# Optimization experiments

Measured on AMD Instinct MI355X. Metric: run time of the kernel, lower is better.

The kernel has to match this reference:

```python
import jax, jax.numpy as jnp
import numpy as np

B, N, C, H = 2, 2048, 1024, 16
D = C // H  # head_dim = 64
ROPE_THETA = 500000.0
INIT_STD = 0.02


def setup_inputs() -> dict:
    key = jax.random.key(0)
    ks = jax.random.split(key, 6)
    hidden_states = jax.random.normal(ks[0], (B, N, C), dtype=jnp.float32)
    # rotary embeddings: standard llama-style, built from rope_theta
    inv_freq = jnp.asarray(1.0 / (ROPE_THETA ** (np.arange(0, D, 2, dtype=np.float32) / D)), jnp.float32)
    freqs = jnp.outer(jnp.arange(N, dtype=jnp.float32), inv_freq)  # (N, D/2)
    emb = jnp.concatenate([freqs, freqs], axis=-1)  # (N, D)
    cos = jnp.broadcast_to(jnp.cos(emb)[None], (B, N, D))
    sin = jnp.broadcast_to(jnp.sin(emb)[None], (B, N, D))
    Wq = jax.random.normal(ks[1], (C, C), jnp.float32) * INIT_STD
    Wk = jax.random.normal(ks[2], (C, C), jnp.float32) * INIT_STD
    Wv = jax.random.normal(ks[3], (C, C), jnp.float32) * INIT_STD
    Wo = jax.random.normal(ks[4], (C, C), jnp.float32) * INIT_STD
    return {"hidden_states": hidden_states, "cos": cos, "sin": sin,
            "Wq": Wq, "Wk": Wk, "Wv": Wv, "Wo": Wo}


def _rotate_half(x):
    x1, x2 = x[..., : D // 2], x[..., D // 2 :]
    return jnp.concatenate((-x2, x1), axis=-1)


def reference(hidden_states, cos, sin, Wq, Wk, Wv, Wo):
    scaling = D ** -0.5
    # projections; W stored as (in, out) so y = x @ W
    q = (hidden_states @ Wq) * scaling
    k = hidden_states @ Wk
    v = hidden_states @ Wv
    q = q.reshape(B, N, H, D)
    k = k.reshape(B, N, H, D)
    v = v.reshape(B, N, H, D)
    # RoPE, cos/sin broadcast over heads: (B,N,1,D)
    c = cos[:, :, None, :]
    s = sin[:, :, None, :]
    q = q * c + _rotate_half(q) * s
    k = k * c + _rotate_half(k) * s
    # causal SDPA (q already scaled)
    scores = jnp.einsum("bqhd,bkhd->bhqk", q, k)  # (B,H,N,N)
    causal = jnp.tril(jnp.ones((N, N), dtype=bool))
    scores = jnp.where(causal[None, None], scores, jnp.finfo(scores.dtype).min)
    probs = jax.nn.softmax(scores, axis=-1)
    out = jnp.einsum("bhqk,bkhd->bqhd", probs, v).reshape(B, N, C)
    return out @ Wo
```

## Files before the change

kernel.cpp:

```cpp
#include <hip/hip_runtime.h>
#include <hip/hip_bf16.h>

typedef __hip_bfloat16 bf16;
typedef __attribute__((ext_vector_type(8))) short short8;
typedef __attribute__((ext_vector_type(4))) short short4v;
typedef __attribute__((ext_vector_type(4))) float f32x4;

#define BB 2
#define NN 2048
#define CC 1024
#define HH 16
#define DD 64
#define MM (BB*NN)
#define QKVN 3072
#define LOG2E 1.44269504088896340736f

__device__ __forceinline__ void glds16(const void* g, void* l) {
    __builtin_amdgcn_global_load_lds((const __attribute__((address_space(1))) void*)g,
                                     (__attribute__((address_space(3))) void*)l, 16, 0, 0);
}
__device__ __forceinline__ short pkbf(float x) { bf16 t = (bf16)x; return *(short*)&t; }

__global__ __launch_bounds__(256) void convert_f32_bf16(const float* __restrict__ in,
                                                        bf16* __restrict__ out) {
    int i = blockIdx.x * 256 + threadIdx.x;
    float4 v = ((const float4*)in)[i];
    short4v s;
    s.x = pkbf(v.x); s.y = pkbf(v.y); s.z = pkbf(v.z); s.w = pkbf(v.w);
    *((short4v*)out + i) = s;
}

__global__ __launch_bounds__(256) void transpose4(const float* __restrict__ W0,
                                                  const float* __restrict__ W1,
                                                  const float* __restrict__ W2,
                                                  const float* __restrict__ W3,
                                                  bf16* __restrict__ Wtqkv,
                                                  bf16* __restrict__ Wto) {
    __shared__ float t[32][33];
    const int z = blockIdx.z;
    const float* W = z == 0 ? W0 : (z == 1 ? W1 : (z == 2 ? W2 : W3));
    bf16* dst = z < 3 ? Wtqkv + (size_t)z * CC * CC : Wto;
    const int tx = threadIdx.x, ty = threadIdx.y;
    const int x0 = blockIdx.x * 32, y0 = blockIdx.y * 32;
    #pragma unroll
    for (int i = 0; i < 4; ++i)
        t[ty + i * 8][tx] = W[(size_t)(y0 + ty + i * 8) * CC + x0 + tx];
    __syncthreads();
    #pragma unroll
    for (int i = 0; i < 4; ++i)
        dst[(size_t)(x0 + ty + i * 8) * CC + y0 + tx] = (bf16)t[tx][ty + i * 8];
}

template<int Nn, int MODE>
__global__ __launch_bounds__(256) void gemm3(const bf16* __restrict__ A,
                                             const bf16* __restrict__ Bt,
                                             void* __restrict__ Cout,
                                             const float* __restrict__ cosp,
                                             const float* __restrict__ sinp,
                                             bf16* __restrict__ VtOut) {
    __shared__ __align__(16) bf16 As[2][128 * 32];
    __shared__ __align__(16) bf16 Bs[2][128 * 32];
    const int tid = threadIdx.x, lane = tid & 63, wid = tid >> 6;
    const int wr = wid >> 1, wc = wid & 1, l16 = lane & 15, lg = lane >> 4;
    const int n0 = blockIdx.x * 128, m0 = blockIdx.y * 128;

    f32x4 acc[4][4];
    #pragma unroll
    for (int i = 0; i < 4; ++i)
        #pragma unroll
        for (int j = 0; j < 4; ++j) acc[i][j] = {0.f, 0.f, 0.f, 0.f};

    const int issue0 = wid * 2;
    const int sr0 = (issue0 * 1024 + lane * 16) >> 6;
    const int sc0 = ((issue0 * 1024 + lane * 16) & 63) >> 1;
    const int sr1 = ((issue0 + 1) * 1024 + lane * 16) >> 6;
    const int sc1 = (((issue0 + 1) * 1024 + lane * 16) & 63) >> 1;

    auto stage = [&](int k0, int bufi) {
        glds16(&A [(size_t)(m0 + sr0) * 1024 + k0 + sc0], (char*)&As[bufi][0] + issue0 * 1024);
        glds16(&Bt[(size_t)(n0 + sr0) * 1024 + k0 + sc0], (char*)&Bs[bufi][0] + issue0 * 1024);
        glds16(&A [(size_t)(m0 + sr1) * 1024 + k0 + sc1], (char*)&As[bufi][0] + (issue0 + 1) * 1024);
        glds16(&Bt[(size_t)(n0 + sr1) * 1024 + k0 + sc1], (char*)&Bs[bufi][0] + (issue0 + 1) * 1024);
    };

    stage(0, 0);
    for (int t = 0; t < 32; ++t) {
        const int cur = t & 1;
        __syncthreads();
        if (t + 1 < 32) stage((t + 1) * 32, cur ^ 1);
        short8 af[4], bfr[4];
        #pragma unroll
        for (int i = 0; i < 4; ++i) af[i]  = *(const short8*)((char*)&As[cur][0] + (wr * 64 + i * 16 + l16) * 64 + lg * 16);
        #pragma unroll
        for (int j = 0; j < 4; ++j) bfr[j] = *(const short8*)((char*)&Bs[cur][0] + (wc * 64 + j * 16 + l16) * 64 + lg * 16);
        #pragma unroll
        for (int i = 0; i < 4; ++i)
            #pragma unroll
            for (int j = 0; j < 4; ++j)
                acc[i][j] = __builtin_amdgcn_mfma_f32_16x16x32_bf16(af[i], bfr[j], acc[i][j], 0, 0, 0);
    }

    if (MODE == 1 && n0 >= 2 * CC) {
        #pragma unroll
        for (int i = 0; i < 4; ++i) {
            const int row0 = m0 + wr * 64 + i * 16 + lg * 4;
            const int bb = row0 >> 11, nn_ = row0 & (NN - 1);
            #pragma unroll
            for (int j = 0; j < 4; ++j) {
                const int col = n0 - 2 * CC + wc * 64 + j * 16 + l16;
                const int hh = col >> 6, d = col & 63;
                short4v s4;
                #pragma unroll
                for (int r = 0; r < 4; ++r) s4[r] = pkbf(acc[i][j][r]);
                *(short4v*)&VtOut[((size_t)(bb * HH + hh) * DD + d) * NN + nn_] = s4;
            }
        }
    } else if (MODE == 1) {
        const float qs = (n0 < CC) ? 0.125f * LOG2E : 1.0f;
        bf16* Cb = (bf16*)Cout;
        #pragma unroll
        for (int i = 0; i < 4; ++i)
            #pragma unroll
            for (int r = 0; r < 4; ++r) {
                const int row = m0 + wr * 64 + i * 16 + lg * 4 + r;
                #pragma unroll
                for (int j = 0; j < 2; ++j) {
                    const int d = j * 16 + l16;
                    const float cv = cosp[(size_t)row * DD + d];
                    const float sv = sinp[(size_t)row * DD + d];
                    const float x1 = acc[i][j][r];
                    const float x2 = acc[i][j + 2][r];
                    const size_t cbase = (size_t)row * QKVN + n0 + wc * 64 + j * 16 + l16;
                    Cb[cbase]      = (bf16)((x1 * cv - x2 * sv) * qs);
                    Cb[cbase + 32] = (bf16)((x2 * cv + x1 * sv) * qs);
                }
            }
    } else {
        float* Cf = (float*)Cout;
        #pragma unroll
        for (int i = 0; i < 4; ++i)
            #pragma unroll
            for (int r = 0; r < 4; ++r) {
                const int row = m0 + wr * 64 + i * 16 + lg * 4 + r;
                #pragma unroll
                for (int j = 0; j < 4; ++j)
                    Cf[(size_t)row * Nn + n0 + wc * 64 + j * 16 + l16] = acc[i][j][r];
            }
    }
}

__global__ __launch_bounds__(256) void flash_mfma3(const bf16* __restrict__ QKV,
                                                   const bf16* __restrict__ Vt,
                                                   bf16* __restrict__ Ab) {
    __shared__ __align__(16) bf16 Ks[2][4096];
    __shared__ __align__(16) bf16 Vs[2][4096];
    const int tid = threadIdx.x, lane = tid & 63, wid = tid >> 6;
    const int l16 = lane & 15, lg = lane >> 4;
    const int bid = blockIdx.x;
    const int bh = bid & 31;
    const int qt = 31 - (bid >> 5);
    const int h = bh & (HH - 1), b = bh >> 4;
    const int wq0 = qt * 64 + wid * 16;
    const int nkt = qt + 1;

    const bf16* Kbase = QKV + (size_t)b * NN * QKVN + CC + h * DD;
    const bf16* Vbase = Vt + (size_t)(b * HH + h) * DD * NN;

    short8 qf[2];
    #pragma unroll
    for (int ch = 0; ch < 2; ++ch)
        qf[ch] = *(const short8*)&QKV[(size_t)(b * NN + wq0 + l16) * QKVN
                                      + h * DD + ch * 32 + lg * 8];

    f32x4 o[4];
    #pragma unroll
    for (int dn = 0; dn < 4; ++dn) o[dn] = {0.f, 0.f, 0.f, 0.f};
    float mx = -1e30f, ls = 0.f;

    auto stage = [&](int kt, int bufi) {
        const int k0s = kt * 64;
        #pragma unroll
        for (int ii = 0; ii < 2; ++ii) {
            const int issue = wid * 2 + ii;
            const int a = issue * 1024 + lane * 16;
            const int r = a >> 7;
            const int cb = (a & 127) ^ ((r & 7) << 4);
            glds16(Kbase + (size_t)(k0s + r) * QKVN + (cb >> 1), (char*)&Ks[bufi][0] + issue * 1024);
            glds16(Vbase + (size_t)r * NN + k0s + (cb >> 1),     (char*)&Vs[bufi][0] + issue * 1024);
        }
    };

    stage(0, 0);
    __syncthreads();

    for (int kt = 0; kt < nkt; ++kt) {
        const int k0 = kt * 64;
        const int cur = kt & 1;
        if (kt + 1 < nkt) stage(kt + 1, cur ^ 1);

        f32x4 st[4];
        #pragma unroll
        for (int kc = 0; kc < 4; ++kc) st[kc] = {0.f, 0.f, 0.f, 0.f};
        __builtin_amdgcn_s_setprio(1);
        #pragma unroll
        for (int kc = 0; kc < 4; ++kc) {
            const int row = kc * 16 + l16;
            const char* rb = (const char*)&Ks[cur][0] + row * 128;
            const int sw = (row & 7) << 4;
            short8 kf0 = *(const short8*)(rb + ((lg * 16) ^ sw));
            short8 kf1 = *(const short8*)(rb + ((64 + lg * 16) ^ sw));
            st[kc] = __builtin_amdgcn_mfma_f32_16x16x32_bf16(kf0, qf[0], st[kc], 0, 0, 0);
            st[kc] = __builtin_amdgcn_mfma_f32_16x16x32_bf16(kf1, qf[1], st[kc], 0, 0, 0);
        }
        __builtin_amdgcn_s_setprio(0);

        if (kt == qt) {
            #pragma unroll
            for (int kc = 0; kc < 4; ++kc)
                #pragma unroll
                for (int r = 0; r < 4; ++r)
                    if (k0 + kc * 16 + lg * 4 + r > wq0 + l16) st[kc][r] = -1e30f;
        }

        float rm = fmaxf(fmaxf(st[0][0], st[0][1]), fmaxf(st[0][2], st[0][3]));
        #pragma unroll
        for (int kc = 1; kc < 4; ++kc)
            rm = fmaxf(rm, fmaxf(fmaxf(st[kc][0], st[kc][1]), fmaxf(st[kc][2], st[kc][3])));
        rm = fmaxf(rm, __shfl_xor(rm, 16, 64));
        rm = fmaxf(rm, __shfl_xor(rm, 32, 64));
        if (__any(rm > mx + 8.0f)) {
            const float mn = fmaxf(mx, rm);
            const float sc = exp2f(mx - mn);
            ls *= sc;
            #pragma unroll
            for (int dn = 0; dn < 4; ++dn) {
                o[dn][0] *= sc; o[dn][1] *= sc; o[dn][2] *= sc; o[dn][3] *= sc;
            }
            mx = mn;
        }
        float rs = 0.f;
        #pragma unroll
        for (int kc = 0; kc < 4; ++kc)
            #pragma unroll
            for (int r = 0; r < 4; ++r) {
                const float p = exp2f(st[kc][r] - mx);
                st[kc][r] = p; rs += p;
            }
        rs += __shfl_xor(rs, 16, 64);
        rs += __shfl_xor(rs, 32, 64);
        ls += rs;

        __builtin_amdgcn_s_setprio(1);
        #pragma unroll
        for (int kc = 0; kc < 4; ++kc) {
            short4v pf;
            pf[0] = pkbf(st[kc][0]); pf[1] = pkbf(st[kc][1]);
            pf[2] = pkbf(st[kc][2]); pf[3] = pkbf(st[kc][3]);
            #pragma unroll
            for (int dn = 0; dn < 4; ++dn) {
                const int row = dn * 16 + l16;
                short4v vf = *(const short4v*)((const char*)&Vs[cur][0] + row * 128
                                               + ((kc * 32 + lg * 8) ^ ((row & 7) << 4)));
                o[dn] = __builtin_amdgcn_mfma_f32_16x16x16bf16_1k(vf, pf, o[dn], 0, 0, 0);
            }
        }
        __builtin_amdgcn_s_setprio(0);

        __syncthreads();
    }

    const float inv = 1.f / ls;
    const size_t rowb = (size_t)(b * NN + wq0 + l16) * CC + h * DD;
    #pragma unroll
    for (int dn = 0; dn < 4; ++dn) {
        short4v s4;
        s4[0] = pkbf(o[dn][0] * inv); s4[1] = pkbf(o[dn][1] * inv);
        s4[2] = pkbf(o[dn][2] * inv); s4[3] = pkbf(o[dn][3] * inv);
        *(short4v*)&Ab[rowb + dn * 16 + lg * 4] = s4;
    }
}

extern "C" void kernel_launch(void* const* d_in, const int* in_sizes, int n_in,
                              void* d_out, int out_size, void* d_ws, size_t ws_size,
                              hipStream_t stream) {
    const float* hs   = (const float*)d_in[0];
    const float* cosp = (const float*)d_in[1];
    const float* sinp = (const float*)d_in[2];
    const float* Wq   = (const float*)d_in[3];
    const float* Wk   = (const float*)d_in[4];
    const float* Wv   = (const float*)d_in[5];
    const float* Wo   = (const float*)d_in[6];
    float* out = (float*)d_out;

    char* ws = (char*)d_ws;
    bf16* hsb   = (bf16*)(ws);
    bf16* Wtqkv = (bf16*)(ws + (8  << 20));
    bf16* Wto   = (bf16*)(ws + (14 << 20));
    bf16* QKV   = (bf16*)(ws + (16 << 20));
    bf16* Vtb   = (bf16*)(ws + (40 << 20));
    bf16* Abuf  = hsb;

    convert_f32_bf16<<<MM * CC / 1024, 256, 0, stream>>>(hs, hsb);

    transpose4<<<dim3(32, 32, 4), dim3(32, 8), 0, stream>>>(Wq, Wk, Wv, Wo, Wtqkv, Wto);

    gemm3<QKVN, 1><<<dim3(QKVN / 128, MM / 128), 256, 0, stream>>>(
        hsb, Wtqkv, QKV, cosp, sinp, Vtb);

    flash_mfma3<<<1024, 256, 0, stream>>>(QKV, Vtb, Abuf);

    gemm3<CC, 2><<<dim3(CC / 128, MM / 128), 256, 0, stream>>>(
        Abuf, Wto, out, nullptr, nullptr, nullptr);
}
```

Baseline: 133.4 us.

## Split flash attention KV range in two blocks and merge partials

Each query tile's key range is split into two halves handled by separate blocks (2048 blocks instead of 1024), each writing unnormalized bf16 partial outputs plus running max and sum. A new merge kernel combines the two halves with rescaling weights. The aim is better load balance and occupancy for the causal triangle. The exchange is an extra kernel launch, an extra pass over the partial outputs, and bf16 rounding of unnormalized partials. The change also uses the hardware exp2 intrinsic and incremental pointer staging with the barrier moved to the top of the loop.

```diff
diff --git a/kernel.cpp b/kernel.cpp
--- a/kernel.cpp
+++ b/kernel.cpp
@@ -20,6 +20,9 @@
                                      (__attribute__((address_space(3))) void*)l, 16, 0, 0);
 }
 __device__ __forceinline__ short pkbf(float x) { bf16 t = (bf16)x; return *(short*)&t; }
+__device__ __forceinline__ float b2f(short s) {
+    return __uint_as_float(((unsigned)(unsigned short)s) << 16);
+}
 
 __global__ __launch_bounds__(256) void convert_f32_bf16(const float* __restrict__ in,
                                                         bf16* __restrict__ out) {
@@ -149,19 +152,27 @@
     }
 }
 
-__global__ __launch_bounds__(256) void flash_mfma3(const bf16* __restrict__ QKV,
+__global__ __launch_bounds__(256) void flash_mfma4(const bf16* __restrict__ QKV,
                                                    const bf16* __restrict__ Vt,
-                                                   bf16* __restrict__ Ab) {
+                                                   bf16* __restrict__ PartA,
+                                                   bf16* __restrict__ PartB,
+                                                   float2* __restrict__ Mlb) {
     __shared__ __align__(16) bf16 Ks[2][4096];
     __shared__ __align__(16) bf16 Vs[2][4096];
     const int tid = threadIdx.x, lane = tid & 63, wid = tid >> 6;
     const int l16 = lane & 15, lg = lane >> 4;
     const int bid = blockIdx.x;
     const int bh = bid & 31;
-    const int qt = 31 - (bid >> 5);
+    const int slot = bid >> 5;
+    const int qt = 31 - (slot >> 1);
+    const int half = slot & 1;
     const int h = bh & (HH - 1), b = bh >> 4;
     const int wq0 = qt * 64 + wid * 16;
     const int nkt = qt + 1;
+    const int hf = (nkt + 1) >> 1;
+    const int t0 = half ? hf : 0;
+    const int cnt = (half ? nkt : hf) - t0;
+    const int grow = b * NN + wq0 + l16;
 
     const bf16* Kbase = QKV + (size_t)b * NN * QKVN + CC + h * DD;
     const bf16* Vbase = Vt + (size_t)(b * HH + h) * DD * NN;
@@ -169,34 +180,38 @@
     short8 qf[2];
     #pragma unroll
     for (int ch = 0; ch < 2; ++ch)
-        qf[ch] = *(const short8*)&QKV[(size_t)(b * NN + wq0 + l16) * QKVN
-                                      + h * DD + ch * 32 + lg * 8];
+        qf[ch] = *(const short8*)&QKV[(size_t)grow * QKVN + h * DD + ch * 32 + lg * 8];
 
     f32x4 o[4];
     #pragma unroll
     for (int dn = 0; dn < 4; ++dn) o[dn] = {0.f, 0.f, 0.f, 0.f};
     float mx = -1e30f, ls = 0.f;
 
-    auto stage = [&](int kt, int bufi) {
-        const int k0s = kt * 64;
-        #pragma unroll
-        for (int ii = 0; ii < 2; ++ii) {
-            const int issue = wid * 2 + ii;
-            const int a = issue * 1024 + lane * 16;
-            const int r = a >> 7;
-            const int cb = (a & 127) ^ ((r & 7) << 4);
-            glds16(Kbase + (size_t)(k0s + r) * QKVN + (cb >> 1), (char*)&Ks[bufi][0] + issue * 1024);
-            glds16(Vbase + (size_t)r * NN + k0s + (cb >> 1),     (char*)&Vs[bufi][0] + issue * 1024);
-        }
+    const int a0 = (wid * 2) * 1024 + lane * 16, a1 = a0 + 1024;
+    const int r0 = a0 >> 7, c0 = ((a0 & 127) ^ ((r0 & 7) << 4)) >> 1;
+    const int r1 = a1 >> 7, c1 = ((a1 & 127) ^ ((r1 & 7) << 4)) >> 1;
+    const bf16* kp0 = Kbase + (size_t)(t0 * 64 + r0) * QKVN + c0;
+    const bf16* kp1 = Kbase + (size_t)(t0 * 64 + r1) * QKVN + c1;
+    const bf16* vp0 = Vbase + (size_t)r0 * NN + t0 * 64 + c0;
+    const bf16* vp1 = Vbase + (size_t)r1 * NN + t0 * 64 + c1;
+    char* ldsK = (char*)&Ks[0][0] + wid * 2048;
+    char* ldsV = (char*)&Vs[0][0] + wid * 2048;
+
+    auto stage = [&](int par) {
+        glds16(kp0, ldsK + par * 8192);
+        glds16(kp1, ldsK + par * 8192 + 1024);
+        glds16(vp0, ldsV + par * 8192);
+        glds16(vp1, ldsV + par * 8192 + 1024);
+        kp0 += 64 * QKVN; kp1 += 64 * QKVN; vp0 += 64; vp1 += 64;
     };
 
-    stage(0, 0);
-    __syncthreads();
-
-    for (int kt = 0; kt < nkt; ++kt) {
+    if (cnt > 0) stage(0);
+    for (int i = 0; i < cnt; ++i) {
+        __syncthreads();
+        if (i + 1 < cnt) stage((i + 1) & 1);
+        const int cur = i & 1;
+        const int kt = t0 + i;
         const int k0 = kt * 64;
-        const int cur = kt & 1;
-        if (kt + 1 < nkt) stage(kt + 1, cur ^ 1);
 
         f32x4 st[4];
         #pragma unroll
@@ -230,7 +245,7 @@
         rm = fmaxf(rm, __shfl_xor(rm, 32, 64));
         if (__any(rm > mx + 8.0f)) {
             const float mn = fmaxf(mx, rm);
-            const float sc = exp2f(mx - mn);
+            const float sc = __builtin_amdgcn_exp2f(mx - mn);
             ls *= sc;
             #pragma unroll
             for (int dn = 0; dn < 4; ++dn) {
@@ -243,7 +258,7 @@
         for (int kc = 0; kc < 4; ++kc)
             #pragma unroll
             for (int r = 0; r < 4; ++r) {
-                const float p = exp2f(st[kc][r] - mx);
+                const float p = __builtin_amdgcn_exp2f(st[kc][r] - mx);
                 st[kc][r] = p; rs += p;
             }
         rs += __shfl_xor(rs, 16, 64);
@@ -265,19 +280,42 @@
             }
         }
         __builtin_amdgcn_s_setprio(0);
-
-        __syncthreads();
     }
 
-    const float inv = 1.f / ls;
-    const size_t rowb = (size_t)(b * NN + wq0 + l16) * CC + h * DD;
+    if (lg == 0) Mlb[((size_t)(half * MM) + grow) * HH + h] = make_float2(mx, ls);
+    bf16* dst = half ? PartB : PartA;
+    const size_t rowb = (size_t)grow * CC + h * DD;
     #pragma unroll
     for (int dn = 0; dn < 4; ++dn) {
         short4v s4;
-        s4[0] = pkbf(o[dn][0] * inv); s4[1] = pkbf(o[dn][1] * inv);
-        s4[2] = pkbf(o[dn][2] * inv); s4[3] = pkbf(o[dn][3] * inv);
-        *(short4v*)&Ab[rowb + dn * 16 + lg * 4] = s4;
+        s4[0] = pkbf(o[dn][0]); s4[1] = pkbf(o[dn][1]);
+        s4[2] = pkbf(o[dn][2]); s4[3] = pkbf(o[dn][3]);
+        *(short4v*)&dst[rowb + dn * 16 + lg * 4] = s4;
     }
+}
+
+__global__ __launch_bounds__(256) void merge_halves(const bf16* __restrict__ pa,
+                                                    const bf16* __restrict__ pb,
+                                                    const float2* __restrict__ ml,
+                                                    bf16* __restrict__ outp) {
+    const int idx = blockIdx.x * 256 + threadIdx.x;
+    const int row = idx >> 7;
+    const int h = (idx & 127) >> 3;
+    const float2 a = ml[(size_t)row * HH + h];
+    const float2 bb = ml[((size_t)MM + row) * HH + h];
+    const float M = fmaxf(a.x, bb.x);
+    const float w0 = __builtin_amdgcn_exp2f(a.x - M);
+    const float w1 = (bb.y > 0.f) ? __builtin_amdgcn_exp2f(bb.x - M) : 0.f;
+    const float inv = 1.f / (a.y * w0 + bb.y * w1);
+    const float f0 = w0 * inv, f1 = w1 * inv;
+    const size_t off = (size_t)idx * 8;
+    short8 va = *(const short8*)(pa + off);
+    short8 vb = *(const short8*)(pb + off);
+    short8 ov;
+    #pragma unroll
+    for (int e = 0; e < 8; ++e)
+        ov[e] = pkbf(b2f(va[e]) * f0 + b2f(vb[e]) * f1);
+    *(short8*)(outp + off) = ov;
 }
 
 extern "C" void kernel_launch(void* const* d_in, const int* in_sizes, int n_in,
@@ -299,6 +337,8 @@
     bf16* QKV   = (bf16*)(ws + (16 << 20));
     bf16* Vtb   = (bf16*)(ws + (40 << 20));
     bf16* Abuf  = hsb;
+    float2* Mlb = (float2*)Wtqkv;
+    bf16* PartB = (bf16*)out;
 
     convert_f32_bf16<<<MM * CC / 1024, 256, 0, stream>>>(hs, hsb);
 
@@ -307,7 +347,9 @@
     gemm3<QKVN, 1><<<dim3(QKVN / 128, MM / 128), 256, 0, stream>>>(
         hsb, Wtqkv, QKV, cosp, sinp, Vtb);
 
-    flash_mfma3<<<1024, 256, 0, stream>>>(QKV, Vtb, Abuf);
+    flash_mfma4<<<2048, 256, 0, stream>>>(QKV, Vtb, Abuf, PartB, Mlb);
+
+    merge_halves<<<2048, 256, 0, stream>>>(Abuf, PartB, Mlb, Abuf);
 
     gemm3<CC, 2><<<dim3(CC / 128, MM / 128), 256, 0, stream>>>(
         Abuf, Wto, out, nullptr, nullptr, nullptr);
```

After: 129.3 us. 3.1% less time.
